# Kernel tuning notes

Measured on AMD Instinct MI355X. Metric: run time of the kernel, lower is better.

The kernel has to match this reference:

```python
import jax, jax.numpy as jnp
import numpy as np

EPS = 1e-8  # F.cosine_similarity default eps
THRESHOLD = 0.5
NUM_PROTOTYPES = 64
W_DIV_ZP = 1.0
W_DIV_PZ = 1.0
W_DIV_PP = 1.0
W_NUM = 1.0
W_CLUSTER = 1.0
W_SEP = 1.0  # NOTE: original forward applies this weight to cluster_loss (upstream bug), replicated here


def setup_inputs() -> dict:
    key = jax.random.key(0)
    k1, k2, k3, k4, k5 = jax.random.split(key, 5)
    N, IN_DIM, P, D = 4096, 768, NUM_PROTOTYPES, 256
    x = jax.random.normal(k1, (N, IN_DIM), dtype=jnp.float32)
    labels = jax.random.randint(k2, (N,), 0, 2, dtype=jnp.int64)
    # nn.Linear(input_dim, prototype_dim): W stored as [D, IN] in torch; use [IN, D] for x @ W
    bound = 1.0 / np.sqrt(IN_DIM)
    W = jax.random.uniform(k3, (IN_DIM, D), minval=-bound, maxval=bound, dtype=jnp.float32)
    b = jax.random.uniform(k4, (D,), minval=-bound, maxval=bound, dtype=jnp.float32)
    prototypes = jax.random.normal(k5, (P, D), dtype=jnp.float32)
    return {"x": x, "labels": labels, "W": W, "b": b, "prototypes": prototypes}


def _cdist(a, b):
    # Euclidean pairwise distances [Na, Nb]
    d2 = (jnp.sum(a * a, -1)[:, None] + jnp.sum(b * b, -1)[None, :]
          - 2.0 * (a @ b.T))
    return jnp.sqrt(jnp.maximum(d2, 0.0))


def _forward(x, labels, W, b, prototypes):
    P = prototypes.shape[0]
    P_pos = P // 2
    z = x @ W + b  # [N, D]

    zn = z / jnp.maximum(jnp.linalg.norm(z, axis=-1, keepdims=True), EPS)
    pn = prototypes / jnp.maximum(jnp.linalg.norm(prototypes, axis=-1, keepdims=True), EPS)
    cos = zn @ pn.T  # [N, P] cosine similarities

    token_sequences = cos[:, :, None] * prototypes[None, :, :]  # [N, P, D]

    dist = _cdist(z, prototypes)  # [N, P]

    # diversity_loss_z_p: nearest sample per prototype
    ni = jnp.argmin(dist, axis=0)  # [P]
    l_zp = jnp.mean(jnp.linalg.norm(z[ni] - prototypes, axis=-1))

    # diversity_loss_p_z: nearest prototype per sample (intended semantics)
    nj = jnp.argmin(dist, axis=1)  # [N]
    l_pz = jnp.mean(jnp.linalg.norm(z - prototypes[nj], axis=-1))

    # diversity_loss_p_p: mean pairwise prototype distance excluding diagonal
    pp = _cdist(prototypes, prototypes)
    off = 1.0 - jnp.eye(P, dtype=pp.dtype)
    l_pp = jnp.sum(pp * off) / (P * (P - 1))

    # loss_num_prototypes: penalize samples similar to > P/4 prototypes
    num_sim = jnp.sum((cos > THRESHOLD).astype(jnp.float32), axis=1)
    l_num = jnp.sum((num_sim > P / 4).astype(jnp.float32))

    # cluster_loss: 1 - max similarity to own-class prototypes, mean over all samples
    max_pos = jnp.max(cos[:, :P_pos], axis=1)
    max_neg = jnp.max(cos[:, P_pos:], axis=1)
    d_cl = jnp.where(labels == 1, 1.0 - max_pos, 1.0 - max_neg)
    l_cluster = jnp.mean(d_cl)

    loss = (W_DIV_ZP * l_zp + W_DIV_PZ * l_pz + W_DIV_PP * l_pp
            + W_NUM * l_num + W_CLUSTER * l_cluster + W_SEP * l_cluster)
    return token_sequences, loss


def reference(x, labels, W, b, prototypes):
    return _forward(x, labels, W, b, prototypes)
```

## Files before the change

kernel.cpp:

```cpp
#include <hip/hip_runtime.h>
#include <hip/hip_bf16.h>

#define NS 4096
#define IND 768
#define PP 64
#define DD 256
#define EPSF 1e-8f
#define KHALF 384

__global__ void k_proto(const float* __restrict__ protos, float* __restrict__ pnorm,
                        float* __restrict__ ppsum, unsigned int* __restrict__ minu,
                        float* __restrict__ accum) {
    int p = blockIdx.x;
    int q = threadIdx.x;
    float s = 0.f;
    for (int d = q; d < DD; d += 64) { float v = protos[p * DD + d]; s += v * v; }
    float t = s;
#pragma unroll
    for (int o = 1; o < 64; o <<= 1) t += __shfl_xor(t, o);
    if (q == 0) pnorm[p] = sqrtf(t);

    float s2 = 0.f;
    for (int d = 0; d < DD; ++d) {
        float diff = protos[p * DD + d] - protos[q * DD + d];
        s2 += diff * diff;
    }
    float dd = (q == p) ? 0.f : sqrtf(s2);
#pragma unroll
    for (int o = 1; o < 64; o <<= 1) dd += __shfl_xor(dd, o);
    if (q == 0) {
        ppsum[p] = dd;
        minu[p] = 0xFFFFFFFFu;
        if (p == 0) { accum[0] = 0.f; accum[1] = 0.f; accum[2] = 0.f; }
    }
}

__global__ __launch_bounds__(256) void k_gemm(const float* __restrict__ x,
                                              const float* __restrict__ W,
                                              float* __restrict__ z0,
                                              float* __restrict__ z1) {
    __shared__ float As[16][68];
    __shared__ float Bs[16][68];
    int tid = threadIdx.x;
    int tx = tid & 15, ty = tid >> 4;
    int m0 = blockIdx.x * 64, n0 = blockIdx.y * 64;
    int kbase = blockIdx.z * KHALF;
    float* __restrict__ zout = blockIdx.z ? z1 : z0;
    float c[4][4] = {};
    for (int k0 = 0; k0 < KHALF; k0 += 16) {
        {
            int k = tid & 15;
            int mb = tid >> 4;
#pragma unroll
            for (int r = 0; r < 4; ++r) {
                int m = mb + r * 16;
                As[k][m] = x[(m0 + m) * IND + kbase + k0 + k];
            }
            int n = tid & 63;
            int kb = tid >> 6;
#pragma unroll
            for (int r = 0; r < 4; ++r) {
                int k2 = kb + r * 4;
                Bs[k2][n] = W[(kbase + k0 + k2) * DD + n0 + n];
            }
        }
        __syncthreads();
#pragma unroll
        for (int k = 0; k < 16; ++k) {
            float a[4], bb[4];
#pragma unroll
            for (int i = 0; i < 4; ++i) a[i] = As[k][ty * 4 + i];
#pragma unroll
            for (int j = 0; j < 4; ++j) bb[j] = Bs[k][tx * 4 + j];
#pragma unroll
            for (int i = 0; i < 4; ++i)
#pragma unroll
                for (int j = 0; j < 4; ++j) c[i][j] += a[i] * bb[j];
        }
        __syncthreads();
    }
#pragma unroll
    for (int i = 0; i < 4; ++i) {
        int m = m0 + ty * 4 + i;
#pragma unroll
        for (int j = 0; j < 4; ++j) zout[m * DD + n0 + tx * 4 + j] = c[i][j];
    }
}

__global__ __launch_bounds__(256) void k_cosw(const float* __restrict__ z0,
                                              const float* __restrict__ z1,
                                              const float* __restrict__ bias,
                                              const float* __restrict__ protos,
                                              const float* __restrict__ pnorm,
                                              const int* __restrict__ labels,
                                              float* __restrict__ out,
                                              unsigned int* __restrict__ minu,
                                              float* __restrict__ accum) {
    __shared__ float protoT[PP * DD];
    __shared__ __align__(16) float rowbuf[4][4][DD];
    int tid = threadIdx.x;
    for (int idx = tid; idx < PP * DD; idx += 256) {
        int p = idx >> 8, d = idx & 255;
        protoT[d * 64 + (p ^ (d & 31))] = protos[idx];
    }

    int w = tid >> 6, lane = tid & 63;
    int p = lane;
    float pn = pnorm[p];
    float pn2 = pn * pn;
    float4 b4 = ((const float4*)bias)[lane];
    int nbase = blockIdx.x * 16 + w * 4;

    float zn[4];
#pragma unroll
    for (int s = 0; s < 4; ++s) {
        int n = nbase + s;
        float4 a = ((const float4*)z0)[n * 64 + lane];
        float4 c = ((const float4*)z1)[n * 64 + lane];
        float4 r;
        r.x = a.x + c.x + b4.x; r.y = a.y + c.y + b4.y;
        r.z = a.z + c.z + b4.z; r.w = a.w + c.w + b4.w;
        float ss = r.x * r.x + r.y * r.y + r.z * r.z + r.w * r.w;
#pragma unroll
        for (int o = 1; o < 64; o <<= 1) ss += __shfl_xor(ss, o);
        zn[s] = sqrtf(ss);
        ((float4*)rowbuf[w][s])[lane] = r;
    }
    __syncthreads();

    float dot0 = 0.f, dot1 = 0.f, dot2 = 0.f, dot3 = 0.f;
#pragma unroll 8
    for (int d4 = 0; d4 < 64; ++d4) {
        float4 r0 = ((const float4*)rowbuf[w][0])[d4];
        float4 r1 = ((const float4*)rowbuf[w][1])[d4];
        float4 r2 = ((const float4*)rowbuf[w][2])[d4];
        float4 r3 = ((const float4*)rowbuf[w][3])[d4];
        int d = d4 * 4;
        float p0 = protoT[(d + 0) * 64 + (p ^ ((d + 0) & 31))];
        float p1 = protoT[(d + 1) * 64 + (p ^ ((d + 1) & 31))];
        float p2 = protoT[(d + 2) * 64 + (p ^ ((d + 2) & 31))];
        float p3 = protoT[(d + 3) * 64 + (p ^ ((d + 3) & 31))];
        dot0 += r0.x * p0 + r0.y * p1 + r0.z * p2 + r0.w * p3;
        dot1 += r1.x * p0 + r1.y * p1 + r1.z * p2 + r1.w * p3;
        dot2 += r2.x * p0 + r2.y * p1 + r2.z * p2 + r2.w * p3;
        dot3 += r3.x * p0 + r3.y * p1 + r3.z * p2 + r3.w * p3;
    }
    float dots[4] = {dot0, dot1, dot2, dot3};

    float cosv[4];
    float regmin = 3.4e38f;
    float s_pz = 0.f, s_cl = 0.f, s_num = 0.f;
#pragma unroll
    for (int s = 0; s < 4; ++s) {
        int n = nbase + s;
        float dot = dots[s];
        float c = dot / (fmaxf(zn[s], EPSF) * fmaxf(pn, EPSF));
        cosv[s] = c;
        float d2 = zn[s] * zn[s] + pn2 - 2.f * dot;
        float dist = sqrtf(fmaxf(d2, 0.f));
        regmin = fminf(regmin, dist);

        unsigned long long bal = __ballot(c > 0.5f);
        int cnt = __popcll(bal);

        float mind = dist;
#pragma unroll
        for (int o = 1; o < 64; o <<= 1) mind = fminf(mind, __shfl_xor(mind, o));
        float mx = c;
#pragma unroll
        for (int o = 1; o < 32; o <<= 1) mx = fmaxf(mx, __shfl_xor(mx, o));
        float max_pos = __shfl(mx, 0);
        float max_neg = __shfl(mx, 32);
        if (lane == 0) {
            float dcl = (labels[n] == 1) ? (1.f - max_pos) : (1.f - max_neg);
            s_pz += mind;
            s_cl += dcl;
            if (cnt > 16) s_num += 1.f;
        }
    }
    atomicMin(&minu[p], __float_as_uint(regmin));
    if (lane == 0) {
        atomicAdd(&accum[0], s_pz);
        atomicAdd(&accum[1], s_cl);
        atomicAdd(&accum[2], s_num);
    }

    const float4* pr4 = (const float4*)protos;
#pragma unroll
    for (int s = 0; s < 4; ++s) {
        int n = nbase + s;
        float4* o4 = (float4*)out + (size_t)n * 4096 + lane;
        float cv = cosv[s];
#pragma unroll 4
        for (int pp = 0; pp < 64; ++pp) {
            float c = __shfl(cv, pp);
            float4 v = pr4[pp * 64 + lane];
            float4 r;
            r.x = c * v.x; r.y = c * v.y; r.z = c * v.z; r.w = c * v.w;
            o4[pp * 64] = r;
        }
    }
}

__global__ void k_final(const unsigned int* __restrict__ minu,
                        const float* __restrict__ ppsum,
                        const float* __restrict__ accum,
                        float* __restrict__ out, int out_last) {
    int lane = threadIdx.x;
    float v = __uint_as_float(minu[lane]) / (float)PP
            + ppsum[lane] / (float)(PP * (PP - 1));
#pragma unroll
    for (int o = 1; o < 64; o <<= 1) v += __shfl_xor(v, o);
    if (lane == 0) {
        float l_pz = accum[0] / (float)NS;
        float l_cl = accum[1] / (float)NS;
        float l_num = accum[2];
        out[out_last] = v + l_pz + l_num + 2.f * l_cl;
    }
}

extern "C" void kernel_launch(void* const* d_in, const int* in_sizes, int n_in,
                              void* d_out, int out_size, void* d_ws, size_t ws_size,
                              hipStream_t stream) {
    const float* x      = (const float*)d_in[0];
    const int*   labels = (const int*)d_in[1];
    const float* W      = (const float*)d_in[2];
    const float* bias   = (const float*)d_in[3];
    const float* protos = (const float*)d_in[4];
    float* out = (float*)d_out;
    float* ws = (float*)d_ws;

    float* z0    = ws;
    float* z1    = ws + 1048576;
    float* pnorm = ws + 2097152;
    float* ppsum = pnorm + 64;
    unsigned int* minu = (unsigned int*)(ppsum + 64);
    float* accum = (float*)(minu + 64);

    k_proto<<<64, 64, 0, stream>>>(protos, pnorm, ppsum, minu, accum);
    dim3 ggrid(64, 4, 2);
    k_gemm<<<ggrid, 256, 0, stream>>>(x, W, z0, z1);
    k_cosw<<<256, 256, 0, stream>>>(z0, z1, bias, protos, pnorm, labels, out, minu, accum);
    k_final<<<1, 64, 0, stream>>>(minu, ppsum, accum, out, out_size - 1);
}
```

Before: 364.3 us.

## Fuse prototype prep into GEMM launch, fold final reduction into cos kernel

Merges the prototype-norm and pairwise-distance kernel into the GEMM launch as extra blocks, and moves the final loss reduction into the last-finishing cos block using a completion counter, cutting four launches to two. The GEMM gains register prefetch of the next k-tile. The cos kernel doubles its grid with two rows per wave, reduces atomics per block through shared memory, and writes the large token output with nontemporal stores. These changes target launch overhead, atomic contention and cache pollution, at the cost of redundant shared-memory prototype loads per block and a more fragile last-block handshake.

```diff
diff --git a/kernel.cpp b/kernel.cpp
--- a/kernel.cpp
+++ b/kernel.cpp
@@ -1,5 +1,4 @@
 #include <hip/hip_runtime.h>
-#include <hip/hip_bf16.h>
 
 #define NS 4096
 #define IND 768
@@ -8,63 +7,84 @@
 #define EPSF 1e-8f
 #define KHALF 384
 
-__global__ void k_proto(const float* __restrict__ protos, float* __restrict__ pnorm,
-                        float* __restrict__ ppsum, unsigned int* __restrict__ minu,
-                        float* __restrict__ accum) {
-    int p = blockIdx.x;
-    int q = threadIdx.x;
-    float s = 0.f;
-    for (int d = q; d < DD; d += 64) { float v = protos[p * DD + d]; s += v * v; }
-    float t = s;
-#pragma unroll
-    for (int o = 1; o < 64; o <<= 1) t += __shfl_xor(t, o);
-    if (q == 0) pnorm[p] = sqrtf(t);
-
-    float s2 = 0.f;
-    for (int d = 0; d < DD; ++d) {
-        float diff = protos[p * DD + d] - protos[q * DD + d];
-        s2 += diff * diff;
-    }
-    float dd = (q == p) ? 0.f : sqrtf(s2);
-#pragma unroll
-    for (int o = 1; o < 64; o <<= 1) dd += __shfl_xor(dd, o);
-    if (q == 0) {
-        ppsum[p] = dd;
-        minu[p] = 0xFFFFFFFFu;
-        if (p == 0) { accum[0] = 0.f; accum[1] = 0.f; accum[2] = 0.f; }
-    }
-}
-
-__global__ __launch_bounds__(256) void k_gemm(const float* __restrict__ x,
-                                              const float* __restrict__ W,
-                                              float* __restrict__ z0,
-                                              float* __restrict__ z1) {
+typedef float f32x4 __attribute__((ext_vector_type(4)));
+
+__global__ __launch_bounds__(256) void k_pre(const float* __restrict__ x,
+                                             const float* __restrict__ W,
+                                             const float* __restrict__ protos,
+                                             float* __restrict__ z0,
+                                             float* __restrict__ z1,
+                                             float* __restrict__ pnorm,
+                                             float* __restrict__ ppsum,
+                                             unsigned int* __restrict__ minu,
+                                             float* __restrict__ accum) {
     __shared__ float As[16][68];
     __shared__ float Bs[16][68];
     int tid = threadIdx.x;
+    int bid = blockIdx.x;
+
+    if (bid >= 512) {
+        int p = bid - 512;
+        int lane = tid & 63, w = tid >> 6;
+        if (w == 0) {
+            float s = 0.f;
+            for (int d = lane; d < DD; d += 64) { float v = protos[p * DD + d]; s += v * v; }
+#pragma unroll
+            for (int o = 1; o < 64; o <<= 1) s += __shfl_xor(s, o);
+            if (lane == 0) pnorm[p] = sqrtf(s);
+        }
+        int q = tid >> 2, quarter = tid & 3;
+        const float* pr = protos + p * DD + quarter * 64;
+        const float* qr = protos + q * DD + quarter * 64;
+        float s2 = 0.f;
+        for (int d = 0; d < 64; ++d) { float diff = pr[d] - qr[d]; s2 += diff * diff; }
+        s2 += __shfl_xor(s2, 1);
+        s2 += __shfl_xor(s2, 2);
+        float contrib = (quarter == 0 && q != p) ? sqrtf(s2) : 0.f;
+#pragma unroll
+        for (int o = 1; o < 64; o <<= 1) contrib += __shfl_xor(contrib, o);
+        float* red = &As[0][0];
+        if (lane == 0) red[w] = contrib;
+        __syncthreads();
+        if (tid == 0) {
+            ppsum[p] = red[0] + red[1] + red[2] + red[3];
+            minu[p] = 0xFFFFFFFFu;
+            if (p == 0) {
+                accum[0] = 0.f; accum[1] = 0.f; accum[2] = 0.f;
+                ((unsigned int*)accum)[3] = 0u;
+            }
+        }
+        return;
+    }
+
+    int bx = bid & 63, by = (bid >> 6) & 3, bz = bid >> 8;
+    int m0 = bx * 64, n0 = by * 64, kbase = bz * KHALF;
+    float* __restrict__ zout = bz ? z1 : z0;
+    float c[4][4] = {};
     int tx = tid & 15, ty = tid >> 4;
-    int m0 = blockIdx.x * 64, n0 = blockIdx.y * 64;
-    int kbase = blockIdx.z * KHALF;
-    float* __restrict__ zout = blockIdx.z ? z1 : z0;
-    float c[4][4] = {};
+    int ka = tid & 15, mb = tid >> 4;
+    int nb = tid & 63, kb = tid >> 6;
+    const float* xp = x + (size_t)(m0 + mb) * IND + kbase + ka;
+    const float* wp = W + (size_t)(kbase + kb) * DD + n0 + nb;
+
+    float ra[4], rb[4];
+#pragma unroll
+    for (int r = 0; r < 4; ++r) ra[r] = xp[r * 16 * IND];
+#pragma unroll
+    for (int r = 0; r < 4; ++r) rb[r] = wp[(size_t)(r * 4) * DD];
+
     for (int k0 = 0; k0 < KHALF; k0 += 16) {
-        {
-            int k = tid & 15;
-            int mb = tid >> 4;
-#pragma unroll
-            for (int r = 0; r < 4; ++r) {
-                int m = mb + r * 16;
-                As[k][m] = x[(m0 + m) * IND + kbase + k0 + k];
-            }
-            int n = tid & 63;
-            int kb = tid >> 6;
-#pragma unroll
-            for (int r = 0; r < 4; ++r) {
-                int k2 = kb + r * 4;
-                Bs[k2][n] = W[(kbase + k0 + k2) * DD + n0 + n];
-            }
-        }
+#pragma unroll
+        for (int r = 0; r < 4; ++r) As[ka][mb + r * 16] = ra[r];
+#pragma unroll
+        for (int r = 0; r < 4; ++r) Bs[kb + r * 4][nb] = rb[r];
         __syncthreads();
+        if (k0 + 16 < KHALF) {
+#pragma unroll
+            for (int r = 0; r < 4; ++r) ra[r] = xp[k0 + 16 + r * 16 * IND];
+#pragma unroll
+            for (int r = 0; r < 4; ++r) rb[r] = wp[(size_t)(k0 + 16 + r * 4) * DD];
+        }
 #pragma unroll
         for (int k = 0; k < 16; ++k) {
             float a[4], bb[4];
@@ -83,7 +103,7 @@
     for (int i = 0; i < 4; ++i) {
         int m = m0 + ty * 4 + i;
 #pragma unroll
-        for (int j = 0; j < 4; ++j) zout[m * DD + n0 + tx * 4 + j] = c[i][j];
+        for (int j = 0; j < 4; ++j) zout[(size_t)m * DD + n0 + tx * 4 + j] = c[i][j];
     }
 }
 
@@ -95,9 +115,13 @@
                                               const int* __restrict__ labels,
                                               float* __restrict__ out,
                                               unsigned int* __restrict__ minu,
-                                              float* __restrict__ accum) {
+                                              float* __restrict__ accum,
+                                              const float* __restrict__ ppsum,
+                                              int out_last) {
     __shared__ float protoT[PP * DD];
-    __shared__ __align__(16) float rowbuf[4][4][DD];
+    __shared__ __align__(16) float rowbuf[4][2][DD];
+    __shared__ float wmin[4][64];
+    __shared__ float wacc[4][3];
     int tid = threadIdx.x;
     for (int idx = tid; idx < PP * DD; idx += 256) {
         int p = idx >> 8, d = idx & 255;
@@ -109,17 +133,17 @@
     float pn = pnorm[p];
     float pn2 = pn * pn;
     float4 b4 = ((const float4*)bias)[lane];
-    int nbase = blockIdx.x * 16 + w * 4;
-
-    float zn[4];
-#pragma unroll
-    for (int s = 0; s < 4; ++s) {
+    int nbase = blockIdx.x * 8 + w * 2;
+
+    float zn[2];
+#pragma unroll
+    for (int s = 0; s < 2; ++s) {
         int n = nbase + s;
         float4 a = ((const float4*)z0)[n * 64 + lane];
-        float4 c = ((const float4*)z1)[n * 64 + lane];
+        float4 cc = ((const float4*)z1)[n * 64 + lane];
         float4 r;
-        r.x = a.x + c.x + b4.x; r.y = a.y + c.y + b4.y;
-        r.z = a.z + c.z + b4.z; r.w = a.w + c.w + b4.w;
+        r.x = a.x + cc.x + b4.x; r.y = a.y + cc.y + b4.y;
+        r.z = a.z + cc.z + b4.z; r.w = a.w + cc.w + b4.w;
         float ss = r.x * r.x + r.y * r.y + r.z * r.z + r.w * r.w;
 #pragma unroll
         for (int o = 1; o < 64; o <<= 1) ss += __shfl_xor(ss, o);
@@ -128,13 +152,11 @@
     }
     __syncthreads();
 
-    float dot0 = 0.f, dot1 = 0.f, dot2 = 0.f, dot3 = 0.f;
+    float dot0 = 0.f, dot1 = 0.f;
 #pragma unroll 8
     for (int d4 = 0; d4 < 64; ++d4) {
         float4 r0 = ((const float4*)rowbuf[w][0])[d4];
         float4 r1 = ((const float4*)rowbuf[w][1])[d4];
-        float4 r2 = ((const float4*)rowbuf[w][2])[d4];
-        float4 r3 = ((const float4*)rowbuf[w][3])[d4];
         int d = d4 * 4;
         float p0 = protoT[(d + 0) * 64 + (p ^ ((d + 0) & 31))];
         float p1 = protoT[(d + 1) * 64 + (p ^ ((d + 1) & 31))];
@@ -142,16 +164,14 @@
         float p3 = protoT[(d + 3) * 64 + (p ^ ((d + 3) & 31))];
         dot0 += r0.x * p0 + r0.y * p1 + r0.z * p2 + r0.w * p3;
         dot1 += r1.x * p0 + r1.y * p1 + r1.z * p2 + r1.w * p3;
-        dot2 += r2.x * p0 + r2.y * p1 + r2.z * p2 + r2.w * p3;
-        dot3 += r3.x * p0 + r3.y * p1 + r3.z * p2 + r3.w * p3;
-    }
-    float dots[4] = {dot0, dot1, dot2, dot3};
-
-    float cosv[4];
+    }
+    float dots[2] = {dot0, dot1};
+
+    float cosv[2];
     float regmin = 3.4e38f;
     float s_pz = 0.f, s_cl = 0.f, s_num = 0.f;
 #pragma unroll
-    for (int s = 0; s < 4; ++s) {
+    for (int s = 0; s < 2; ++s) {
         int n = nbase + s;
         float dot = dots[s];
         float c = dot / (fmaxf(zn[s], EPSF) * fmaxf(pn, EPSF));
@@ -178,44 +198,52 @@
             if (cnt > 16) s_num += 1.f;
         }
     }
-    atomicMin(&minu[p], __float_as_uint(regmin));
-    if (lane == 0) {
-        atomicAdd(&accum[0], s_pz);
-        atomicAdd(&accum[1], s_cl);
-        atomicAdd(&accum[2], s_num);
+
+    wmin[w][lane] = regmin;
+    if (lane == 0) { wacc[w][0] = s_pz; wacc[w][1] = s_cl; wacc[w][2] = s_num; }
+    __syncthreads();
+    if (w == 0) {
+        float m = fminf(fminf(wmin[0][lane], wmin[1][lane]),
+                        fminf(wmin[2][lane], wmin[3][lane]));
+        atomicMin(&minu[lane], __float_as_uint(m));
+        if (lane == 0) {
+            atomicAdd(&accum[0], wacc[0][0] + wacc[1][0] + wacc[2][0] + wacc[3][0]);
+            atomicAdd(&accum[1], wacc[0][1] + wacc[1][1] + wacc[2][1] + wacc[3][1]);
+            atomicAdd(&accum[2], wacc[0][2] + wacc[1][2] + wacc[2][2] + wacc[3][2]);
+        }
+        __threadfence();
+        unsigned int t = 0;
+        if (lane == 0) t = atomicAdd((unsigned int*)accum + 3, 1u);
+        t = __shfl(t, 0);
+        if (t == 511u) {
+            __threadfence();
+            float mv = __uint_as_float(atomicMin(&minu[lane], 0xFFFFFFFFu));
+            float v = mv * (1.f / PP) + ppsum[lane] * (1.f / (PP * (PP - 1)));
+#pragma unroll
+            for (int o = 1; o < 64; o <<= 1) v += __shfl_xor(v, o);
+            if (lane == 0) {
+                float l_pz = atomicAdd(&accum[0], 0.f) * (1.f / NS);
+                float l_cl = atomicAdd(&accum[1], 0.f) * (1.f / NS);
+                float l_num = atomicAdd(&accum[2], 0.f);
+                out[out_last] = v + l_pz + l_num + 2.f * l_cl;
+            }
+        }
     }
 
     const float4* pr4 = (const float4*)protos;
 #pragma unroll
-    for (int s = 0; s < 4; ++s) {
+    for (int s = 0; s < 2; ++s) {
         int n = nbase + s;
-        float4* o4 = (float4*)out + (size_t)n * 4096 + lane;
+        f32x4* o4 = (f32x4*)out + (size_t)n * 4096 + lane;
         float cv = cosv[s];
 #pragma unroll 4
         for (int pp = 0; pp < 64; ++pp) {
             float c = __shfl(cv, pp);
             float4 v = pr4[pp * 64 + lane];
-            float4 r;
+            f32x4 r;
             r.x = c * v.x; r.y = c * v.y; r.z = c * v.z; r.w = c * v.w;
-            o4[pp * 64] = r;
-        }
-    }
-}
-
-__global__ void k_final(const unsigned int* __restrict__ minu,
-                        const float* __restrict__ ppsum,
-                        const float* __restrict__ accum,
-                        float* __restrict__ out, int out_last) {
-    int lane = threadIdx.x;
-    float v = __uint_as_float(minu[lane]) / (float)PP
-            + ppsum[lane] / (float)(PP * (PP - 1));
-#pragma unroll
-    for (int o = 1; o < 64; o <<= 1) v += __shfl_xor(v, o);
-    if (lane == 0) {
-        float l_pz = accum[0] / (float)NS;
-        float l_cl = accum[1] / (float)NS;
-        float l_num = accum[2];
-        out[out_last] = v + l_pz + l_num + 2.f * l_cl;
+            __builtin_nontemporal_store(r, &o4[pp * 64]);
+        }
     }
 }
 
@@ -237,9 +265,7 @@
     unsigned int* minu = (unsigned int*)(ppsum + 64);
     float* accum = (float*)(minu + 64);
 
-    k_proto<<<64, 64, 0, stream>>>(protos, pnorm, ppsum, minu, accum);
-    dim3 ggrid(64, 4, 2);
-    k_gemm<<<ggrid, 256, 0, stream>>>(x, W, z0, z1);
-    k_cosw<<<256, 256, 0, stream>>>(z0, z1, bias, protos, pnorm, labels, out, minu, accum);
-    k_final<<<1, 64, 0, stream>>>(minu, ppsum, accum, out, out_size - 1);
+    k_pre<<<576, 256, 0, stream>>>(x, W, protos, z0, z1, pnorm, ppsum, minu, accum);
+    k_cosw<<<512, 256, 0, stream>>>(z0, z1, bias, protos, pnorm, labels, out,
+                                    minu, accum, ppsum, out_size - 1);
 }
```

New measurement: 350.3 us. 3.8% less time.
